# Performance work log

Hardware: AMD Instinct MI355X
Metric: run time of the kernel (lower is better)

Reference implementation:

```python
import jax, jax.numpy as jnp
import numpy as np
import math

B, S, H, NH = 4, 1024, 1024, 16
DH = H // NH
G = 100  # native graph size


def setup_inputs() -> dict:
    key = jax.random.key(0)
    ks = jax.random.split(key, 12)
    sc = 1.0 / math.sqrt(H)
    return {
        "v": jax.random.normal(ks[0], (B, S, H), jnp.float32),
        "k": jax.random.normal(ks[1], (B, S, H), jnp.float32),
        "q": jax.random.normal(ks[2], (B, S, H), jnp.float32),
        "mask": jax.random.randint(ks[3], (B, 1, 1, S), 0, 2) == 1,
        "graph": jax.random.uniform(ks[4], (B, G, G), jnp.float32),
        "Wq": jax.random.normal(ks[5], (H, H), jnp.float32) * sc,
        "bq": jnp.zeros((H,), jnp.float32),
        "Wk": jax.random.normal(ks[6], (H, H), jnp.float32) * sc,
        "bk": jnp.zeros((H,), jnp.float32),
        "Wv": jax.random.normal(ks[7], (H, H), jnp.float32) * sc,
        "bv": jnp.zeros((H,), jnp.float32),
        "Wm": jax.random.normal(ks[8], (H, H), jnp.float32) * sc,
        "bm": jnp.zeros((H,), jnp.float32),
    }


def _heads(x, W, b):
    # [B,S,H] -> [B,NH,S,DH]
    y = x @ W + b
    return y.reshape(B, S, NH, DH).transpose(0, 2, 1, 3)


def reference(v, k, q, mask, graph, Wq, bq, Wk, bk, Wv, bv, Wm, bm):
    qh = _heads(q, Wq, bq)
    kh = _heads(k, Wk, bk)
    vh = _heads(v, Wv, bv)
    scores = jnp.einsum("bhqd,bhkd->bhqk", qh, kh) / math.sqrt(DH)
    # pad 100x100 graph to SxS (zeros outside top-left block), as in torch source
    if S > G:
        graph = jnp.zeros((B, S, S), graph.dtype).at[:, :G, :G].set(graph)
    # scores - scores*graph, then mask fill and softmax
    scores = scores - scores * graph[:, None, :, :]
    scores = jnp.where(mask, jnp.float32(-1e9), scores)
    att = jax.nn.softmax(scores, axis=-1)  # dropout is identity in eval
    out = jnp.einsum("bhqk,bhkd->bhqd", att, vh)
    out = out.transpose(0, 2, 1, 3).reshape(B, S, H)
    return out @ Wm + bm
```

## Files before the change

kernel.cpp:

```cpp
#include <hip/hip_runtime.h>
#include <hip/hip_bf16.h>
#include <cstdio>

#define S_ 1024
#define H_ 1024
#define NH_ 16
#define DH_ 64
#define G_ 100

typedef __attribute__((ext_vector_type(8))) short bf16x8;
typedef __attribute__((ext_vector_type(4))) short bf16x4;
typedef __attribute__((ext_vector_type(4))) float f32x4;

__device__ __forceinline__ f32x4 mfma16(bf16x8 a, bf16x8 b, f32x4 c) {
  return __builtin_amdgcn_mfma_f32_16x16x32_bf16(a, b, c, 0, 0, 0);
}

__device__ __forceinline__ short f2bf(float f) {
  union { float f; unsigned int i; } x;
  x.f = f;
  unsigned int r = x.i + 0x7fff + ((x.i >> 16) & 1);
  return (short)(r >> 16);
}

__device__ __forceinline__ unsigned cvtpk(float lo, float hi) {
  unsigned r;
  asm("v_cvt_pk_bf16_f32 %0, %1, %2" : "=v"(r) : "v"(lo), "v"(hi));
  return r;
}

__device__ __forceinline__ void gload16(const void* g, void* l) {
  __builtin_amdgcn_global_load_lds(
      (const __attribute__((address_space(1))) unsigned int*)g,
      (__attribute__((address_space(3))) unsigned int*)l, 16, 0, 0);
}

__global__ __launch_bounds__(256) void transpose_w(
    const float* __restrict__ W0, const float* __restrict__ W1,
    const float* __restrict__ W2, const float* __restrict__ W3,
    short* __restrict__ T0, short* __restrict__ T1,
    short* __restrict__ T2, short* __restrict__ T3) {
  __shared__ short tile[64][72];
  const float* W = (blockIdx.z == 0) ? W0 : (blockIdx.z == 1) ? W1
                 : (blockIdx.z == 2) ? W2 : W3;
  short* T = (blockIdx.z == 0) ? T0 : (blockIdx.z == 1) ? T1
           : (blockIdx.z == 2) ? T2 : T3;
  const int t = threadIdx.x;
  const int r0 = t >> 3;
  const int c8 = (t & 7) * 8;
  const int kbase = blockIdx.x * 64, nbase = blockIdx.y * 64;
#pragma unroll
  for (int p = 0; p < 2; ++p) {
    int r = p * 32 + r0;
    const float* src = W + (size_t)(kbase + r) * H_ + nbase + c8;
    f32x4 u0 = *reinterpret_cast<const f32x4*>(src);
    f32x4 u1 = *reinterpret_cast<const f32x4*>(src + 4);
#pragma unroll
    for (int j = 0; j < 4; ++j) {
      tile[r][c8 + j] = f2bf(u0[j]);
      tile[r][c8 + 4 + j] = f2bf(u1[j]);
    }
  }
  __syncthreads();
#pragma unroll
  for (int p = 0; p < 2; ++p) {
    int r = p * 32 + r0;
    bf16x8 o;
#pragma unroll
    for (int j = 0; j < 8; ++j) o[j] = tile[c8 + j][r];
    *reinterpret_cast<bf16x8*>(T + (size_t)(nbase + r) * H_ + kbase + c8) = o;
  }
}

__global__ __launch_bounds__(256, 3) void qkv128f(
    const float* __restrict__ A0, const float* __restrict__ A1,
    const float* __restrict__ A2, const short* __restrict__ W0,
    const short* __restrict__ W1, const short* __restrict__ W2,
    const float* __restrict__ b0, const float* __restrict__ b1,
    const float* __restrict__ b2, short* __restrict__ O0,
    short* __restrict__ O1, short* __restrict__ O2) {
  __shared__ float Af[128 * 64];
  __shared__ short Bs[128 * 64];
  const int z = blockIdx.z;
  const float* A  = (z == 0) ? A0 : (z == 1) ? A1 : A2;
  const short* Bt = (z == 0) ? W0 : (z == 1) ? W1 : W2;
  const float* bias = (z == 0) ? b0 : (z == 1) ? b1 : b2;
  short* Cb = (z == 0) ? O0 : (z == 1) ? O1 : O2;
  const float scale = (z == 0) ? 0.125f : 1.0f;
  const int K = H_;
  const int t = threadIdx.x;
  const int l = t & 63, w = t >> 6;
  const int lr = l & 15, lg = l >> 4;
  const int lx = lr & 7;
  const int wm = w >> 1, wn = w & 1;
  const int bm = blockIdx.x * 128, bn = blockIdx.y * 128;
  f32x4 acc[4][4];
#pragma unroll
  for (int i = 0; i < 4; ++i)
#pragma unroll
    for (int j = 0; j < 4; ++j) acc[i][j] = (f32x4){0.f, 0.f, 0.f, 0.f};

  const int ar = t >> 4;
  const int ag = t & 15;
  const int asg = (ag & 8) | ((ag & 7) ^ (ar & 7));
  const float* Ab = A + (size_t)(bm + ar) * K + asg * 4;
  const int br = t >> 3;
  const int bsc = ((t & 7) ^ (br & 7)) * 8;
  const short* Bb = Bt + (size_t)(bn + br) * K + bsc;

  for (int kb = 0; kb < K; kb += 64) {
#pragma unroll
    for (int p = 0; p < 8; ++p)
      gload16(Ab + (size_t)p * 16 * K + kb,
              (char*)Af + p * 4096 + t * 16);
#pragma unroll
    for (int i = 0; i < 4; ++i)
      gload16(Bb + (size_t)i * 32 * K + kb,
              (char*)Bs + i * 4096 + t * 16);
    __syncthreads();
#pragma unroll
    for (int ks = 0; ks < 2; ++ks) {
      bf16x8 af[4], bfr[4];
#pragma unroll
      for (int mi = 0; mi < 4; ++mi) {
        const int row = wm * 64 + mi * 16 + lr;
        const int s0 = (ks * 8) | ((lg * 2) ^ lx);
        f32x4 alo = *reinterpret_cast<const f32x4*>(&Af[row * 64 + s0 * 4]);
        f32x4 ahi =
            *reinterpret_cast<const f32x4*>(&Af[row * 64 + (s0 ^ 1) * 4]);
        union { unsigned u[4]; bf16x8 v; } c;
        c.u[0] = cvtpk(alo[0], alo[1]);
        c.u[1] = cvtpk(alo[2], alo[3]);
        c.u[2] = cvtpk(ahi[0], ahi[1]);
        c.u[3] = cvtpk(ahi[2], ahi[3]);
        af[mi] = c.v;
      }
#pragma unroll
      for (int ni = 0; ni < 4; ++ni)
        bfr[ni] = *reinterpret_cast<const bf16x8*>(
            &Bs[(wn * 64 + ni * 16 + lr) * 64 + (((ks * 4 + lg) ^ lx) * 8)]);
#pragma unroll
      for (int mi = 0; mi < 4; ++mi)
#pragma unroll
        for (int ni = 0; ni < 4; ++ni)
          acc[mi][ni] = mfma16(af[mi], bfr[ni], acc[mi][ni]);
    }
    __syncthreads();
  }
#pragma unroll
  for (int mi = 0; mi < 4; ++mi)
#pragma unroll
    for (int ni = 0; ni < 4; ++ni) {
      int col = bn + wn * 64 + ni * 16 + lr;
      float bv = bias[col];
      int h = col >> 6, d = col & 63;
      if (z == 2) {
        int row0 = bm + wm * 64 + mi * 16 + lg * 4;
        int b = row0 >> 10, s0 = row0 & 1023;
        bf16x4 pk;
#pragma unroll
        for (int r = 0; r < 4; ++r) pk[r] = f2bf(acc[mi][ni][r] + bv);
        *reinterpret_cast<bf16x4*>(
            Cb + (((size_t)(b * NH_ + h)) * DH_ + d) * S_ + s0) = pk;
      } else {
#pragma unroll
        for (int r = 0; r < 4; ++r) {
          int row = bm + wm * 64 + mi * 16 + lg * 4 + r;
          int b = row >> 10, s = row & 1023;
          Cb[(((size_t)(b * NH_ + h)) * S_ + s) * DH_ + d] =
              f2bf((acc[mi][ni][r] + bv) * scale);
        }
      }
    }
}

__global__ __launch_bounds__(256) void out64(
    const short* __restrict__ A, const short* __restrict__ Bt,
    const float* __restrict__ bias, float* __restrict__ Cf) {
  __shared__ short As[64 * 64];
  __shared__ short Bs[128 * 64];
  const int K = H_, N = H_;
  const int t = threadIdx.x;
  const int l = t & 63, w = t >> 6;
  const int lr = l & 15, lg = l >> 4;
  const int lx = lr & 7;
  const int wm = w >> 1, wn = w & 1;
  const int bm = blockIdx.x * 64, bn = blockIdx.y * 128;
  f32x4 acc[2][4];
#pragma unroll
  for (int i = 0; i < 2; ++i)
#pragma unroll
    for (int j = 0; j < 4; ++j) acc[i][j] = (f32x4){0.f, 0.f, 0.f, 0.f};
  const int sr = t >> 3;
  const int ssc = ((t & 7) ^ (sr & 7)) * 8;
  const short* Ab = A + (size_t)(bm + sr) * K + ssc;
  const short* Bb = Bt + (size_t)(bn + sr) * K + ssc;
  short* la = As + t * 8;
  short* lb = Bs + t * 8;

  for (int kb = 0; kb < K; kb += 64) {
#pragma unroll
    for (int i = 0; i < 2; ++i)
      gload16(Ab + (size_t)i * 32 * K + kb, la + i * 2048);
#pragma unroll
    for (int i = 0; i < 4; ++i)
      gload16(Bb + (size_t)i * 32 * K + kb, lb + i * 2048);
    __syncthreads();
#pragma unroll
    for (int ks = 0; ks < 2; ++ks) {
      bf16x8 af[2], bfr[4];
#pragma unroll
      for (int mi = 0; mi < 2; ++mi)
        af[mi] = *reinterpret_cast<const bf16x8*>(
            &As[(wm * 32 + mi * 16 + lr) * 64 + (((ks * 4 + lg) ^ lx) * 8)]);
#pragma unroll
      for (int ni = 0; ni < 4; ++ni)
        bfr[ni] = *reinterpret_cast<const bf16x8*>(
            &Bs[(wn * 64 + ni * 16 + lr) * 64 + (((ks * 4 + lg) ^ lx) * 8)]);
#pragma unroll
      for (int mi = 0; mi < 2; ++mi)
#pragma unroll
        for (int ni = 0; ni < 4; ++ni)
          acc[mi][ni] = mfma16(af[mi], bfr[ni], acc[mi][ni]);
    }
    __syncthreads();
  }
#pragma unroll
  for (int mi = 0; mi < 2; ++mi)
#pragma unroll
    for (int ni = 0; ni < 4; ++ni) {
      int col = bn + wn * 64 + ni * 16 + lr;
      float bv = bias[col];
#pragma unroll
      for (int r = 0; r < 4; ++r) {
        int row = bm + wm * 32 + mi * 16 + lg * 4 + r;
        Cf[(size_t)row * N + col] = acc[mi][ni][r] + bv;
      }
    }
}

__global__ __launch_bounds__(256) void attn(
    const short* __restrict__ Qh, const short* __restrict__ Kh,
    const short* __restrict__ VhT, const float* __restrict__ graph,
    const int* __restrict__ mask, short* __restrict__ ctx) {
  __shared__ short Kb[64 * 64];
  __shared__ short Vb[64 * 64];
  __shared__ short P[4 * 16 * 64];
  __shared__ float maskf[S_];
  const int lin = blockIdx.x;
  const int gid = (lin & 7) * 128 + (lin >> 3);
  const int bh = gid >> 4, qt = gid & 15;
  const int b = bh >> 4, h = bh & 15;
  const int t = threadIdx.x, w = t >> 6, l = t & 63;
  const int lr = l & 15, lg = l >> 4;
  const int lx = lr & 7;
  const int q0 = qt * 64 + w * 16;
  const int qg = q0 + lr;
  short* Pw = P + w * 1024;
  const short* Qrow = Qh + ((size_t)bh * S_ + qg) * DH_;
  bf16x8 qf0 = *reinterpret_cast<const bf16x8*>(Qrow + lg * 8);
  bf16x8 qf1 = *reinterpret_cast<const bf16x8*>(Qrow + 32 + lg * 8);
  f32x4 o[4];
#pragma unroll
  for (int i = 0; i < 4; ++i) o[i] = (f32x4){0.f, 0.f, 0.f, 0.f};
  float llp = 0.f;

  const int rs = t >> 2;
  const int g0 = t & 3;
  const int sw0 = ((g0 ^ (rs & 7)) * 8);
  const int sw1 = (((g0 + 4) ^ (rs & 7)) * 8);
  const short* Ksrc = Kh + ((size_t)bh * S_ + rs) * DH_ + g0 * 8;
  const short* Vsrc = VhT + ((size_t)bh * DH_ + rs) * S_ + g0 * 8;

  {
    int4 mv = reinterpret_cast<const int4*>(mask + b * S_)[t];
    f32x4 mo;
    const float C = -11.0903549f;
    mo.x = mv.x ? -1.0e9f : C;
    mo.y = mv.y ? -1.0e9f : C;
    mo.z = mv.z ? -1.0e9f : C;
    mo.w = mv.w ? -1.0e9f : C;
    reinterpret_cast<f32x4*>(maskf)[t] = mo;
  }
  {
    int4 ka = *reinterpret_cast<const int4*>(Ksrc);
    int4 kb2 = *reinterpret_cast<const int4*>(Ksrc + 32);
    int4 va = *reinterpret_cast<const int4*>(Vsrc);
    int4 vb2 = *reinterpret_cast<const int4*>(Vsrc + 32);
    *reinterpret_cast<int4*>(&Kb[rs * 64 + sw0]) = ka;
    *reinterpret_cast<int4*>(&Kb[rs * 64 + sw1]) = kb2;
    *reinterpret_cast<int4*>(&Vb[rs * 64 + sw0]) = va;
    *reinterpret_cast<int4*>(&Vb[rs * 64 + sw1]) = vb2;
  }
  __syncthreads();

  for (int kc = 0; kc < S_; kc += 64) {
    const bool pf = (kc + 64 < S_);
    int4 ka, kb2, va, vb2;
    if (pf) {
      ka = *reinterpret_cast<const int4*>(Ksrc + (size_t)(kc + 64) * DH_);
      kb2 = *reinterpret_cast<const int4*>(Ksrc + (size_t)(kc + 64) * DH_ + 32);
      va = *reinterpret_cast<const int4*>(Vsrc + kc + 64);
      vb2 = *reinterpret_cast<const int4*>(Vsrc + kc + 64 + 32);
    }
    f32x4 sacc[4];
    __builtin_amdgcn_s_setprio(1);
#pragma unroll
    for (int mf = 0; mf < 4; ++mf) {
      const int rk = mf * 16 + lr;
      bf16x8 k0 = *reinterpret_cast<const bf16x8*>(
          &Kb[rk * 64 + ((lg ^ lx) * 8)]);
      bf16x8 k1 = *reinterpret_cast<const bf16x8*>(
          &Kb[rk * 64 + (((4 + lg) ^ lx) * 8)]);
      f32x4 sa = (f32x4){0.f, 0.f, 0.f, 0.f};
      sa = mfma16(k0, qf0, sa);
      sa = mfma16(k1, qf1, sa);
      sacc[mf] = sa;
    }
    __builtin_amdgcn_s_setprio(0);
    const bool gblk = (q0 < G_) && (kc < G_);
    const int pw0 = lr * 64 + (lg & 1) * 4;
#pragma unroll
    for (int mf = 0; mf < 4; ++mf) {
      f32x4 mk = *reinterpret_cast<const f32x4*>(&maskf[kc + mf * 16 + lg * 4]);
      f32x4 sa = sacc[mf];
      if (gblk) {
#pragma unroll
        for (int r = 0; r < 4; ++r) {
          int kg = kc + mf * 16 + lg * 4 + r;
          if (qg < G_ && kg < G_)
            sa[r] *= (1.f - graph[((size_t)b * G_ + qg) * G_ + kg]);
        }
      }
      float e0 = __expf(sa[0] + mk[0]);
      float e1 = __expf(sa[1] + mk[1]);
      float e2 = __expf(sa[2] + mk[2]);
      float e3 = __expf(sa[3] + mk[3]);
      llp += (e0 + e1) + (e2 + e3);
      int2 pk2;
      pk2.x = (int)cvtpk(e0, e1);
      pk2.y = (int)cvtpk(e2, e3);
      *reinterpret_cast<int2*>(
          &Pw[pw0 + (((2 * mf + (lg >> 1)) ^ lx) * 8)]) = pk2;
    }
    __builtin_amdgcn_s_setprio(1);
#pragma unroll
    for (int ks = 0; ks < 2; ++ks) {
      bf16x8 pa = *reinterpret_cast<const bf16x8*>(
          &Pw[lr * 64 + (((ks * 4 + lg) ^ lx) * 8)]);
#pragma unroll
      for (int nf = 0; nf < 4; ++nf) {
        const int rv = nf * 16 + lr;
        bf16x8 vfr = *reinterpret_cast<const bf16x8*>(
            &Vb[rv * 64 + (((ks * 4 + lg) ^ lx) * 8)]);
        o[nf] = mfma16(pa, vfr, o[nf]);
      }
    }
    __builtin_amdgcn_s_setprio(0);
    if (pf) {
      __syncthreads();
      *reinterpret_cast<int4*>(&Kb[rs * 64 + sw0]) = ka;
      *reinterpret_cast<int4*>(&Kb[rs * 64 + sw1]) = kb2;
      *reinterpret_cast<int4*>(&Vb[rs * 64 + sw0]) = va;
      *reinterpret_cast<int4*>(&Vb[rs * 64 + sw1]) = vb2;
      __syncthreads();
    }
  }
  llp += __shfl_xor(llp, 16);
  llp += __shfl_xor(llp, 32);
  float rinv[4];
#pragma unroll
  for (int r = 0; r < 4; ++r)
    rinv[r] = __builtin_amdgcn_rcpf(__shfl(llp, lg * 4 + r, 64));
#pragma unroll
  for (int nf = 0; nf < 4; ++nf)
#pragma unroll
    for (int r = 0; r < 4; ++r) {
      float val = o[nf][r] * rinv[r];
      ctx[((size_t)b * S_ + q0 + lg * 4 + r) * H_ + h * DH_ + nf * 16 + lr] =
          f2bf(val);
    }
}

extern "C" void kernel_launch(void* const* d_in, const int* in_sizes, int n_in,
                              void* d_out, int out_size, void* d_ws, size_t ws_size,
                              hipStream_t stream) {
  const int B = in_sizes[0] / (S_ * H_);
  const int M = B * S_;
  const float* v    = (const float*)d_in[0];
  const float* k    = (const float*)d_in[1];
  const float* q    = (const float*)d_in[2];
  const int*   mask = (const int*)d_in[3];
  const float* graph= (const float*)d_in[4];
  const float* Wq   = (const float*)d_in[5];
  const float* bq   = (const float*)d_in[6];
  const float* Wk   = (const float*)d_in[7];
  const float* bk   = (const float*)d_in[8];
  const float* Wv   = (const float*)d_in[9];
  const float* bv   = (const float*)d_in[10];
  const float* Wm   = (const float*)d_in[11];
  const float* bm   = (const float*)d_in[12];

  short* ws = (short*)d_ws;
  const size_t WSZ = (size_t)H_ * H_;
  const size_t TSZ = (size_t)M * H_;
  short* WqT = ws;
  short* WkT = ws + WSZ;
  short* WvT = ws + 2 * WSZ;
  short* WmT = ws + 3 * WSZ;
  short* Qh  = ws + 4 * WSZ;
  short* Kh  = Qh + TSZ;
  short* VhT = Kh + TSZ;
  short* ctx = VhT + TSZ;
  if (ws_size < (4 * WSZ + 4 * TSZ) * sizeof(short)) {
    fprintf(stderr, "kernel_launch: ws too small (%zu)\n", ws_size);
    return;
  }

  transpose_w<<<dim3(H_ / 64, H_ / 64, 4), 256, 0, stream>>>(
      Wq, Wk, Wv, Wm, WqT, WkT, WvT, WmT);
  qkv128f<<<dim3(M / 128, H_ / 128, 3), 256, 0, stream>>>(
      q, k, v, WqT, WkT, WvT, bq, bk, bv, Qh, Kh, VhT);
  attn<<<dim3(1024), 256, 0, stream>>>(Qh, Kh, VhT, graph, mask, ctx);
  out64<<<dim3(M / 64, H_ / 128), 256, 0, stream>>>(
      ctx, WmT, bm, (float*)d_out);
}
```

Baseline: 105.5 us.

## Double-buffer LDS tiles in QKV and output projection GEMMs with async prefetch

Both projection GEMM kernels now split K into 32-wide steps and alternate between two LDS buffers. The next tile's global-to-LDS loads are issued before the current tile is computed, with explicit vmcnt waits and raw barriers, so memory latency can overlap MFMA work. The XOR swizzle is adapted to the narrower 32-element rows. The trade-off is twice as many barriers per K, each step doing half the MFMA work, and handwritten waitcnt counts that must match the number of issued loads.

Measured after the change: 111.7 us. +5.9%, slower.

```diff
diff --git a/kernel.cpp b/kernel.cpp
--- a/kernel.cpp
+++ b/kernel.cpp
@@ -79,8 +79,8 @@
     const float* __restrict__ b0, const float* __restrict__ b1,
     const float* __restrict__ b2, short* __restrict__ O0,
     short* __restrict__ O1, short* __restrict__ O2) {
-  __shared__ float Af[128 * 64];
-  __shared__ short Bs[128 * 64];
+  __shared__ float Af[2][128 * 32];
+  __shared__ short Bs[2][128 * 32];
   const int z = blockIdx.z;
   const float* A  = (z == 0) ? A0 : (z == 1) ? A1 : A2;
   const short* Bt = (z == 0) ? W0 : (z == 1) ? W1 : W2;
@@ -92,6 +92,7 @@
   const int l = t & 63, w = t >> 6;
   const int lr = l & 15, lg = l >> 4;
   const int lx = lr & 7;
+  const int lb3 = lr & 3;
   const int wm = w >> 1, wn = w & 1;
   const int bm = blockIdx.x * 128, bn = blockIdx.y * 128;
   f32x4 acc[4][4];
@@ -100,52 +101,62 @@
 #pragma unroll
     for (int j = 0; j < 4; ++j) acc[i][j] = (f32x4){0.f, 0.f, 0.f, 0.f};
 
-  const int ar = t >> 4;
-  const int ag = t & 15;
-  const int asg = (ag & 8) | ((ag & 7) ^ (ar & 7));
-  const float* Ab = A + (size_t)(bm + ar) * K + asg * 4;
-  const int br = t >> 3;
-  const int bsc = ((t & 7) ^ (br & 7)) * 8;
-  const short* Bb = Bt + (size_t)(bn + br) * K + bsc;
-
-  for (int kb = 0; kb < K; kb += 64) {
-#pragma unroll
-    for (int p = 0; p < 8; ++p)
-      gload16(Ab + (size_t)p * 16 * K + kb,
-              (char*)Af + p * 4096 + t * 16);
-#pragma unroll
-    for (int i = 0; i < 4; ++i)
-      gload16(Bb + (size_t)i * 32 * K + kb,
-              (char*)Bs + i * 4096 + t * 16);
-    __syncthreads();
-#pragma unroll
-    for (int ks = 0; ks < 2; ++ks) {
-      bf16x8 af[4], bfr[4];
-#pragma unroll
-      for (int mi = 0; mi < 4; ++mi) {
-        const int row = wm * 64 + mi * 16 + lr;
-        const int s0 = (ks * 8) | ((lg * 2) ^ lx);
-        f32x4 alo = *reinterpret_cast<const f32x4*>(&Af[row * 64 + s0 * 4]);
-        f32x4 ahi =
-            *reinterpret_cast<const f32x4*>(&Af[row * 64 + (s0 ^ 1) * 4]);
-        union { unsigned u[4]; bf16x8 v; } c;
-        c.u[0] = cvtpk(alo[0], alo[1]);
-        c.u[1] = cvtpk(alo[2], alo[3]);
-        c.u[2] = cvtpk(ahi[0], ahi[1]);
-        c.u[3] = cvtpk(ahi[2], ahi[3]);
-        af[mi] = c.v;
-      }
+  const int ar = t >> 3;
+  const float* Ab = A + (size_t)(bm + ar) * K + ((t & 7) ^ (ar & 7)) * 4;
+  const int br = t >> 2;
+  const short* Bb = Bt + (size_t)(bn + br) * K + ((t & 3) ^ (br & 3)) * 8;
+
+  auto stage = [&](int buf, int kb) {
+#pragma unroll
+    for (int p = 0; p < 4; ++p)
+      gload16(Ab + (size_t)p * 32 * K + kb,
+              (char*)&Af[buf][0] + p * 4096 + t * 16);
+#pragma unroll
+    for (int p = 0; p < 2; ++p)
+      gload16(Bb + (size_t)p * 64 * K + kb,
+              (char*)&Bs[buf][0] + p * 4096 + t * 16);
+  };
+
+  stage(0, 0);
+  const int NT = K >> 5;
+  for (int tt = 0; tt < NT; ++tt) {
+    const int cur = tt & 1;
+    if (tt + 1 < NT) {
+      stage(cur ^ 1, (tt + 1) << 5);
+      asm volatile("s_waitcnt vmcnt(6)" ::: "memory");
+    } else {
+      asm volatile("s_waitcnt vmcnt(0)" ::: "memory");
+    }
+    __builtin_amdgcn_s_barrier();
+    asm volatile("" ::: "memory");
+    bf16x8 af[4], bfr[4];
+#pragma unroll
+    for (int mi = 0; mi < 4; ++mi) {
+      const int row = wm * 64 + mi * 16 + lr;
+      const float* Ar = &Af[cur][row * 32];
+      f32x4 alo = *reinterpret_cast<const f32x4*>(Ar + (((lg * 2) ^ lx) * 4));
+      f32x4 ahi =
+          *reinterpret_cast<const f32x4*>(Ar + (((lg * 2 + 1) ^ lx) * 4));
+      union { unsigned u[4]; bf16x8 v; } c;
+      c.u[0] = cvtpk(alo[0], alo[1]);
+      c.u[1] = cvtpk(alo[2], alo[3]);
+      c.u[2] = cvtpk(ahi[0], ahi[1]);
+      c.u[3] = cvtpk(ahi[2], ahi[3]);
+      af[mi] = c.v;
+    }
+#pragma unroll
+    for (int ni = 0; ni < 4; ++ni) {
+      const int rb = wn * 64 + ni * 16 + lr;
+      bfr[ni] = *reinterpret_cast<const bf16x8*>(
+          &Bs[cur][rb * 32 + ((lg ^ lb3) * 8)]);
+    }
+#pragma unroll
+    for (int mi = 0; mi < 4; ++mi)
 #pragma unroll
       for (int ni = 0; ni < 4; ++ni)
-        bfr[ni] = *reinterpret_cast<const bf16x8*>(
-            &Bs[(wn * 64 + ni * 16 + lr) * 64 + (((ks * 4 + lg) ^ lx) * 8)]);
-#pragma unroll
-      for (int mi = 0; mi < 4; ++mi)
-#pragma unroll
-        for (int ni = 0; ni < 4; ++ni)
-          acc[mi][ni] = mfma16(af[mi], bfr[ni], acc[mi][ni]);
-    }
-    __syncthreads();
+        acc[mi][ni] = mfma16(af[mi], bfr[ni], acc[mi][ni]);
+    asm volatile("" ::: "memory");
+    __builtin_amdgcn_s_barrier();
   }
 #pragma unroll
   for (int mi = 0; mi < 4; ++mi)
@@ -177,13 +188,13 @@
 __global__ __launch_bounds__(256) void out64(
     const short* __restrict__ A, const short* __restrict__ Bt,
     const float* __restrict__ bias, float* __restrict__ Cf) {
-  __shared__ short As[64 * 64];
-  __shared__ short Bs[128 * 64];
+  __shared__ short As[2][64 * 32];
+  __shared__ short Bs[2][128 * 32];
   const int K = H_, N = H_;
   const int t = threadIdx.x;
   const int l = t & 63, w = t >> 6;
   const int lr = l & 15, lg = l >> 4;
-  const int lx = lr & 7;
+  const int lb3 = lr & 3;
   const int wm = w >> 1, wn = w & 1;
   const int bm = blockIdx.x * 64, bn = blockIdx.y * 128;
   f32x4 acc[2][4];
@@ -191,39 +202,49 @@
   for (int i = 0; i < 2; ++i)
 #pragma unroll
     for (int j = 0; j < 4; ++j) acc[i][j] = (f32x4){0.f, 0.f, 0.f, 0.f};
-  const int sr = t >> 3;
-  const int ssc = ((t & 7) ^ (sr & 7)) * 8;
-  const short* Ab = A + (size_t)(bm + sr) * K + ssc;
-  const short* Bb = Bt + (size_t)(bn + sr) * K + ssc;
-  short* la = As + t * 8;
-  short* lb = Bs + t * 8;
-
-  for (int kb = 0; kb < K; kb += 64) {
-#pragma unroll
-    for (int i = 0; i < 2; ++i)
-      gload16(Ab + (size_t)i * 32 * K + kb, la + i * 2048);
-#pragma unroll
-    for (int i = 0; i < 4; ++i)
-      gload16(Bb + (size_t)i * 32 * K + kb, lb + i * 2048);
-    __syncthreads();
-#pragma unroll
-    for (int ks = 0; ks < 2; ++ks) {
-      bf16x8 af[2], bfr[4];
-#pragma unroll
-      for (int mi = 0; mi < 2; ++mi)
-        af[mi] = *reinterpret_cast<const bf16x8*>(
-            &As[(wm * 32 + mi * 16 + lr) * 64 + (((ks * 4 + lg) ^ lx) * 8)]);
+  const int sr = t >> 2;
+  const int sg = ((t & 3) ^ (sr & 3)) * 8;
+  const short* Ab = A + (size_t)(bm + sr) * K + sg;
+  const short* Bb = Bt + (size_t)(bn + sr) * K + sg;
+
+  auto stage = [&](int buf, int kb) {
+    gload16(Ab + kb, (char*)&As[buf][0] + t * 16);
+    gload16(Bb + kb, (char*)&Bs[buf][0] + t * 16);
+    gload16(Bb + (size_t)64 * K + kb, (char*)&Bs[buf][0] + 4096 + t * 16);
+  };
+
+  stage(0, 0);
+  const int NT = K >> 5;
+  for (int tt = 0; tt < NT; ++tt) {
+    const int cur = tt & 1;
+    if (tt + 1 < NT) {
+      stage(cur ^ 1, (tt + 1) << 5);
+      asm volatile("s_waitcnt vmcnt(3)" ::: "memory");
+    } else {
+      asm volatile("s_waitcnt vmcnt(0)" ::: "memory");
+    }
+    __builtin_amdgcn_s_barrier();
+    asm volatile("" ::: "memory");
+    bf16x8 af[2], bfr[4];
+#pragma unroll
+    for (int mi = 0; mi < 2; ++mi) {
+      const int row = wm * 32 + mi * 16 + lr;
+      af[mi] = *reinterpret_cast<const bf16x8*>(
+          &As[cur][row * 32 + ((lg ^ lb3) * 8)]);
+    }
+#pragma unroll
+    for (int ni = 0; ni < 4; ++ni) {
+      const int rb = wn * 64 + ni * 16 + lr;
+      bfr[ni] = *reinterpret_cast<const bf16x8*>(
+          &Bs[cur][rb * 32 + ((lg ^ lb3) * 8)]);
+    }
+#pragma unroll
+    for (int mi = 0; mi < 2; ++mi)
 #pragma unroll
       for (int ni = 0; ni < 4; ++ni)
-        bfr[ni] = *reinterpret_cast<const bf16x8*>(
-            &Bs[(wn * 64 + ni * 16 + lr) * 64 + (((ks * 4 + lg) ^ lx) * 8)]);
-#pragma unroll
-      for (int mi = 0; mi < 2; ++mi)
-#pragma unroll
-        for (int ni = 0; ni < 4; ++ni)
-          acc[mi][ni] = mfma16(af[mi], bfr[ni], acc[mi][ni]);
-    }
-    __syncthreads();
+        acc[mi][ni] = mfma16(af[mi], bfr[ni], acc[mi][ni]);
+    asm volatile("" ::: "memory");
+    __builtin_amdgcn_s_barrier();
   }
 #pragma unroll
   for (int mi = 0; mi < 2; ++mi)
```

## Double-buffer QKV GEMM LDS tiles and use native exp2 in attention softmax

Applied to the files above, without the earlier changes.

The QKV projection GEMM now uses two LDS buffers with a K-step of 32 instead of a single buffer with K-step 64. The next tile's global-to-LDS loads are issued before the MFMAs run, so memory traffic overlaps compute. Separately, the Q scale is folded to include log2(e) and the mask offset constant is rescaled, so the attention kernel can use the raw v_exp_f32 (exp2) instead of __expf. This removes a multiply per element. The smaller K-step doubles the number of barriers per tile, and the exp2 rewrite depends on the fixed offset constant still keeping values in range.

Result: no change. 106.2 us (+0.7%).

```diff
diff --git a/kernel.cpp b/kernel.cpp
--- a/kernel.cpp
+++ b/kernel.cpp
@@ -26,6 +26,12 @@
 __device__ __forceinline__ unsigned cvtpk(float lo, float hi) {
   unsigned r;
   asm("v_cvt_pk_bf16_f32 %0, %1, %2" : "=v"(r) : "v"(lo), "v"(hi));
+  return r;
+}
+
+__device__ __forceinline__ float exp2hw(float x) {
+  float r;
+  asm("v_exp_f32 %0, %1" : "=v"(r) : "v"(x));
   return r;
 }
 
@@ -79,19 +85,20 @@
     const float* __restrict__ b0, const float* __restrict__ b1,
     const float* __restrict__ b2, short* __restrict__ O0,
     short* __restrict__ O1, short* __restrict__ O2) {
-  __shared__ float Af[128 * 64];
-  __shared__ short Bs[128 * 64];
+  __shared__ float Af[2][128 * 32];
+  __shared__ short Bs[2][128 * 32];
   const int z = blockIdx.z;
   const float* A  = (z == 0) ? A0 : (z == 1) ? A1 : A2;
   const short* Bt = (z == 0) ? W0 : (z == 1) ? W1 : W2;
   const float* bias = (z == 0) ? b0 : (z == 1) ? b1 : b2;
   short* Cb = (z == 0) ? O0 : (z == 1) ? O1 : O2;
-  const float scale = (z == 0) ? 0.125f : 1.0f;
+  const float scale = (z == 0) ? 0.18033688f : 1.0f;
   const int K = H_;
   const int t = threadIdx.x;
   const int l = t & 63, w = t >> 6;
   const int lr = l & 15, lg = l >> 4;
   const int lx = lr & 7;
+  const int lb3 = lr & 3;
   const int wm = w >> 1, wn = w & 1;
   const int bm = blockIdx.x * 128, bn = blockIdx.y * 128;
   f32x4 acc[4][4];
@@ -100,51 +107,54 @@
 #pragma unroll
     for (int j = 0; j < 4; ++j) acc[i][j] = (f32x4){0.f, 0.f, 0.f, 0.f};
 
-  const int ar = t >> 4;
-  const int ag = t & 15;
-  const int asg = (ag & 8) | ((ag & 7) ^ (ar & 7));
-  const float* Ab = A + (size_t)(bm + ar) * K + asg * 4;
-  const int br = t >> 3;
-  const int bsc = ((t & 7) ^ (br & 7)) * 8;
-  const short* Bb = Bt + (size_t)(bn + br) * K + bsc;
-
-  for (int kb = 0; kb < K; kb += 64) {
-#pragma unroll
-    for (int p = 0; p < 8; ++p)
-      gload16(Ab + (size_t)p * 16 * K + kb,
-              (char*)Af + p * 4096 + t * 16);
-#pragma unroll
-    for (int i = 0; i < 4; ++i)
-      gload16(Bb + (size_t)i * 32 * K + kb,
-              (char*)Bs + i * 4096 + t * 16);
-    __syncthreads();
-#pragma unroll
-    for (int ks = 0; ks < 2; ++ks) {
-      bf16x8 af[4], bfr[4];
-#pragma unroll
-      for (int mi = 0; mi < 4; ++mi) {
-        const int row = wm * 64 + mi * 16 + lr;
-        const int s0 = (ks * 8) | ((lg * 2) ^ lx);
-        f32x4 alo = *reinterpret_cast<const f32x4*>(&Af[row * 64 + s0 * 4]);
-        f32x4 ahi =
-            *reinterpret_cast<const f32x4*>(&Af[row * 64 + (s0 ^ 1) * 4]);
-        union { unsigned u[4]; bf16x8 v; } c;
-        c.u[0] = cvtpk(alo[0], alo[1]);
-        c.u[1] = cvtpk(alo[2], alo[3]);
-        c.u[2] = cvtpk(ahi[0], ahi[1]);
-        c.u[3] = cvtpk(ahi[2], ahi[3]);
-        af[mi] = c.v;
-      }
+  const int ar = t >> 3;
+  const float* Ab = A + (size_t)(bm + ar) * K + ((t & 7) ^ (ar & 7)) * 4;
+  const int br = t >> 2;
+  const short* Bb = Bt + (size_t)(bn + br) * K + ((t & 3) ^ (br & 3)) * 8;
+
+  auto stage = [&](int buf, int kb) {
+#pragma unroll
+    for (int p = 0; p < 4; ++p)
+      gload16(Ab + (size_t)p * 32 * K + kb,
+              (char*)&Af[buf][0] + p * 4096 + t * 16);
+#pragma unroll
+    for (int p = 0; p < 2; ++p)
+      gload16(Bb + (size_t)p * 64 * K + kb,
+              (char*)&Bs[buf][0] + p * 4096 + t * 16);
+  };
+
+  stage(0, 0);
+  __syncthreads();
+  const int NT = K >> 5;
+  for (int tt = 0; tt < NT; ++tt) {
+    const int cur = tt & 1;
+    bf16x8 af[4], bfr[4];
+#pragma unroll
+    for (int mi = 0; mi < 4; ++mi) {
+      const int row = wm * 64 + mi * 16 + lr;
+      const float* Ar = &Af[cur][row * 32];
+      f32x4 alo = *reinterpret_cast<const f32x4*>(Ar + (((lg * 2) ^ lx) * 4));
+      f32x4 ahi =
+          *reinterpret_cast<const f32x4*>(Ar + (((lg * 2 + 1) ^ lx) * 4));
+      union { unsigned u[4]; bf16x8 v; } c;
+      c.u[0] = cvtpk(alo[0], alo[1]);
+      c.u[1] = cvtpk(alo[2], alo[3]);
+      c.u[2] = cvtpk(ahi[0], ahi[1]);
+      c.u[3] = cvtpk(ahi[2], ahi[3]);
+      af[mi] = c.v;
+    }
+#pragma unroll
+    for (int ni = 0; ni < 4; ++ni) {
+      const int rb = wn * 64 + ni * 16 + lr;
+      bfr[ni] = *reinterpret_cast<const bf16x8*>(
+          &Bs[cur][rb * 32 + ((lg ^ lb3) * 8)]);
+    }
+    if (tt + 1 < NT) stage(cur ^ 1, (tt + 1) << 5);
+#pragma unroll
+    for (int mi = 0; mi < 4; ++mi)
 #pragma unroll
       for (int ni = 0; ni < 4; ++ni)
-        bfr[ni] = *reinterpret_cast<const bf16x8*>(
-            &Bs[(wn * 64 + ni * 16 + lr) * 64 + (((ks * 4 + lg) ^ lx) * 8)]);
-#pragma unroll
-      for (int mi = 0; mi < 4; ++mi)
-#pragma unroll
-        for (int ni = 0; ni < 4; ++ni)
-          acc[mi][ni] = mfma16(af[mi], bfr[ni], acc[mi][ni]);
-    }
+        acc[mi][ni] = mfma16(af[mi], bfr[ni], acc[mi][ni]);
     __syncthreads();
   }
 #pragma unroll
@@ -275,7 +285,7 @@
   {
     int4 mv = reinterpret_cast<const int4*>(mask + b * S_)[t];
     f32x4 mo;
-    const float C = -11.0903549f;
+    const float C = -16.0f;
     mo.x = mv.x ? -1.0e9f : C;
     mo.y = mv.y ? -1.0e9f : C;
     mo.z = mv.z ? -1.0e9f : C;
@@ -332,10 +342,10 @@
             sa[r] *= (1.f - graph[((size_t)b * G_ + qg) * G_ + kg]);
         }
       }
-      float e0 = __expf(sa[0] + mk[0]);
-      float e1 = __expf(sa[1] + mk[1]);
-      float e2 = __expf(sa[2] + mk[2]);
-      float e3 = __expf(sa[3] + mk[3]);
+      float e0 = exp2hw(sa[0] + mk[0]);
+      float e1 = exp2hw(sa[1] + mk[1]);
+      float e2 = exp2hw(sa[2] + mk[2]);
+      float e3 = exp2hw(sa[3] + mk[3]);
       llp += (e0 + e1) + (e2 + e3);
       int2 pk2;
       pk2.x = (int)cvtpk(e0, e1);
```
